# Optimization experiments

Hardware: AMD Instinct MI355X
Metric: run time of the kernel (lower is better)

Reference implementation:

```python
import jax, jax.numpy as jnp
import numpy as np

B = 1024; PAST = 64; FUT = 16; N = PAST + FUT; DM = N // 3; HID = 64
EMB = [(2000, 32), (7, 8), (24, 8)]
OUTP = 3 + 32 + 8 + 8  # 51 = out_preprocess
O = OUTP - 1           # 50
HID1 = 64; HID2 = 64
NEG = -1e30  # finite stand-in for -inf so fully-masked rows stay NaN-free


def _gcnn(x, A, W, act):
    # D = diag((1 + rowsum(sign(relu(A-1e-15))))^-0.5); out = act(D @ A @ D @ (x W^T))
    d = (1.0 + (A > 1e-15).astype(x.dtype).sum(1)) ** -0.5
    An = d[:, None] * A * d[None, :]            # (P,P)
    h = jnp.einsum('pq,bqc->bpc', An, x @ W.T)  # (B,P,out)
    return jax.nn.relu(h) if act else h


def _forward(data, emb0, emb1, emb2, w1, b1, w2, b2, w3, b3,
             M, Wg1a, Wg1b, Wk, smoothing, Wg2a, Wg2b):
    # learned adjacency: masked softmax over strictly-lower-triangular support
    mask = jnp.tril(jnp.ones((N, N), data.dtype), -1)
    A0 = jax.nn.relu(M @ M.T)
    A = jax.nn.softmax(jnp.where(mask > 0, A0, NEG), axis=1)
    A = jnp.where(mask > 0, A, 0.0)
    # pre_processing: embeddings + MLP, then re-append last raw column
    tabs = (emb0, emb1, emb2)
    e = [t[data[:, :, i].astype(jnp.int32)] for i, t in enumerate(tabs)]
    h = jnp.concatenate(e + [data[:, :, -3:]], -1)        # (B,N,51)
    h = jax.nn.relu(h @ w1.T + b1)
    h = jax.nn.relu(h @ w2.T + b2)
    h = h @ w3.T + b3                                      # (B,N,50)
    x = jnp.concatenate([h, data[:, :, -1:]], -1)          # (B,N,51)
    sg1, sg2 = x[:, :PAST], x[:, PAST:]
    A11 = A[:PAST, :PAST]
    x1 = _gcnn(_gcnn(sg1, A11, Wg1a, True), A11, Wg1b, False)   # (B,PAST,50)
    xk = jnp.concatenate([x1, sg2[:, :, :-1]], 1)               # (B,N,50)
    y = x[:, :PAST, -1:]                                        # (B,PAST,1)
    # Kernel: batched Mahalanobis quadratic form (diagonal computed directly)
    xp, xf = xk[:, :PAST], xk[:, PAST:]
    theta = Wk @ Wk.T
    theta = (theta + theta.T) / 2
    diff = xp[:, None, :, :] - xf[:, :, None, :]                # (B,F,P,50)
    q = jnp.einsum('bjip,pq,bjiq->bji', diff, theta, diff)      # (B,F,P)
    alpha = -0.5 * q / (jax.nn.sigmoid(smoothing[0]) * 0.01)
    At = A[FUT:, :PAST] if False else A[PAST:, :PAST]           # (F,P)
    At = jax.nn.softmax(jnp.where(At != 0, At, NEG), axis=1)
    # torch Softmax(dim=1) on (B,F,P) normalizes over the F axis
    alpha = jax.nn.softmax(jnp.where(At[None] >= 0.004, alpha, NEG), axis=1)
    yh = jnp.einsum('bjp,bpo->bjo', alpha, y)                   # (B,F,1)
    x2 = jnp.concatenate([sg2[:, :, :-1], yh], -1)              # (B,F,51)
    A22 = A[PAST:, PAST:]
    out = _gcnn(_gcnn(x2, A22, Wg2a, True), A22, Wg2b, False).reshape(-1, FUT)
    # cdist(x, x), p=2, with NaN-safe sqrt at zero distance
    xc = jnp.concatenate([sg1, x2], 1)                          # (B,N,51)
    sq = jnp.sum(xc * xc, -1)
    d2 = jnp.maximum(sq[:, :, None] + sq[:, None, :]
                     - 2.0 * jnp.einsum('bnc,bmc->bnm', xc, xc), 0.0)
    dist = jnp.where(d2 > 0, jnp.sqrt(jnp.where(d2 > 0, d2, 1.0)), 0.0)
    return (out, dist, A)


def setup_inputs() -> dict:
    key = jax.random.key(0)
    ks = jax.random.split(key, 20)
    cols = [jax.random.randint(ks[i], (B, N, 1), 0, EMB[i][0]).astype(jnp.float32)
            for i in range(3)]
    data = jnp.concatenate(cols + [jax.random.normal(ks[3], (B, N, 3), jnp.float32)], -1)
    g = lambda k, s, sc: jax.random.normal(k, s, jnp.float32) * sc
    return dict(
        data=data,
        emb0=g(ks[4], EMB[0], 1.0),
        emb1=g(ks[5], EMB[1], 1.0),
        emb2=g(ks[6], EMB[2], 1.0),
        w1=g(ks[7], (128, OUTP), OUTP ** -0.5), b1=jnp.zeros((128,), jnp.float32),
        w2=g(ks[8], (128, 128), 128 ** -0.5), b2=jnp.zeros((128,), jnp.float32),
        w3=g(ks[9], (O, 128), 128 ** -0.5), b3=jnp.zeros((O,), jnp.float32),
        M=g(ks[10], (N, DM), 1.0),
        Wg1a=g(ks[11], (HID1, OUTP), OUTP ** -0.5),
        Wg1b=g(ks[12], (O, HID1), HID1 ** -0.5),
        Wk=g(ks[13], (O, HID), 0.05),
        smoothing=g(ks[14], (1,), 1.0),
        Wg2a=g(ks[15], (HID2, OUTP), OUTP ** -0.5),
        Wg2b=g(ks[16], (1, HID2), HID2 ** -0.5),
    )


def reference(data, emb0, emb1, emb2, w1, b1, w2, b2, w3, b3,
              M, Wg1a, Wg1b, Wk, smoothing, Wg2a, Wg2b):
    return _forward(data, emb0, emb1, emb2, w1, b1, w2, b2, w3, b3,
                    M, Wg1a, Wg1b, Wk, smoothing, Wg2a, Wg2b)
```

## Files before the change

### kernel.cpp

```cpp
#include <hip/hip_runtime.h>
#include <math.h>


#define NEGBIG (-1e30f)

#define OFF_X     0
#define OFF_YH    7454720
#define OFF_A     7471104
#define OFF_AN22  7481600
#define OFF_MK    7484356
#define OFF_GAH   7514692
#define OFF_GAL   7516740
#define OFF_G2AT  7521156
#define OFF_SC    7524420
#define OFF_W1H   7524424
#define OFF_W1L   7528520
#define OFF_W2H   7532616
#define OFF_W2L   7540808
#define OFF_W3H   7549000
#define OFF_W3L   7553096
#define OFF_ANH   7557192
#define OFF_ANL   7559240
#define OFF_GBH   7561288
#define OFF_GBL   7563336
#define OFF_WKH   7565384
#define OFF_WKL   7567432

#define OUT_OUT   0
#define OUT_DIST  16384
#define OUT_A     6569984

typedef __attribute__((ext_vector_type(8))) short bf16x8;
typedef __attribute__((ext_vector_type(4))) short s16x4;
typedef __attribute__((ext_vector_type(4))) float f32x4;

__device__ __forceinline__ unsigned short f2bf(float x) {
  union { float f; unsigned u; } v; v.f = x;
  unsigned r = v.u + 0x7fffu + ((v.u >> 16) & 1u);
  return (unsigned short)(r >> 16);
}
__device__ __forceinline__ float bf2f(unsigned short h) {
  union { unsigned u; float f; } v; v.u = ((unsigned)h) << 16; return v.f;
}
__device__ __forceinline__ void split2(float v, unsigned short& h, unsigned short& l) {
  unsigned short hh = f2bf(v);
  h = hh;
  l = f2bf(v - bf2f(hh));
}
#define SWZ6(r, k) (((r) << 6) + (((((k) >> 3) ^ ((r) & 7)) << 3) | ((k) & 7)))
#define SWZ7(r, k) (((r) << 7) + (((((k) >> 3) ^ ((r) & 7)) << 3) | ((k) & 7)))

#define MFMA3(acc, aH, aL, bH, bL) \
  acc = __builtin_amdgcn_mfma_f32_16x16x32_bf16(aH, bH, acc, 0, 0, 0); \
  acc = __builtin_amdgcn_mfma_f32_16x16x32_bf16(aH, bL, acc, 0, 0, 0); \
  acc = __builtin_amdgcn_mfma_f32_16x16x32_bf16(aL, bH, acc, 0, 0, 0);
#define MFMA4(acc, aH, aL, bH, bL) \
  MFMA3(acc, aH, aL, bH, bL) \
  acc = __builtin_amdgcn_mfma_f32_16x16x32_bf16(aL, bL, acc, 0, 0, 0);

__global__ __launch_bounds__(256) void k_prep(
    const float* __restrict__ M, const float* __restrict__ Wk,
    const float* __restrict__ sm,
    const float* __restrict__ w1, const float* __restrict__ w2,
    const float* __restrict__ w3,
    const float* __restrict__ wg1a, const float* __restrict__ wg1b,
    const float* __restrict__ wg2a,
    float* __restrict__ ws, float* __restrict__ out)
{
  __shared__ float Msh[80 * 26];
  __shared__ float Ash[80 * 80];
  __shared__ float d1[64];
  __shared__ float d2s[16];
  const int t = threadIdx.x;

  if (blockIdx.x == 0) {
    for (int e = t; e < 80 * 26; e += 256) Msh[e] = M[e];
    __syncthreads();
    for (int e = t; e < 6400; e += 256) {
      int i = e / 80, j = e % 80;
      float v = 0.f;
      if (j < i) {
        float s = 0.f;
        for (int k = 0; k < 26; ++k) s += Msh[i * 26 + k] * Msh[j * 26 + k];
        v = s > 0.f ? s : 0.f;
      }
      Ash[e] = v;
    }
    __syncthreads();
    if (t > 0 && t < 80) {
      int i = t;
      float m = -3.4e38f;
      for (int j = 0; j < i; ++j) m = fmaxf(m, Ash[i * 80 + j]);
      float s = 0.f;
      for (int j = 0; j < i; ++j) {
        float e = expf(Ash[i * 80 + j] - m);
        Ash[i * 80 + j] = e;
        s += e;
      }
      float inv = 1.f / s;
      for (int j = 0; j < i; ++j) Ash[i * 80 + j] *= inv;
    }
    __syncthreads();
    {
      float* Aws = ws + OFF_A;
      float* Aout = out + OUT_A;
      for (int e = t; e < 6400; e += 256) { Aws[e] = Ash[e]; Aout[e] = Ash[e]; }
    }
    if (t < 64) {
      int c = 0;
      for (int j = 0; j < 64; ++j) if (Ash[t * 80 + j] > 1e-15f) ++c;
      d1[t] = 1.f / sqrtf(1.f + (float)c);
    } else if (t < 80) {
      int i = t - 64; int c = 0;
      for (int j = 0; j < 16; ++j) if (Ash[(64 + i) * 80 + 64 + j] > 1e-15f) ++c;
      d2s[i] = 1.f / sqrtf(1.f + (float)c);
    }
    __syncthreads();
    {
      float* an22 = ws + OFF_AN22;
      unsigned short* anH = (unsigned short*)(ws + OFF_ANH);
      unsigned short* anL = (unsigned short*)(ws + OFF_ANL);
      for (int e = t; e < 4096; e += 256) {
        int i = e >> 6, j = e & 63;
        float v = d1[i] * Ash[i * 80 + j] * d1[j];
        unsigned short h = f2bf(v);
        anH[e] = h; anL[e] = f2bf(v - bf2f(h));
      }
      for (int e = t; e < 256; e += 256) {
        int i = e >> 4, j = e & 15;
        an22[e] = d2s[i] * Ash[(64 + i) * 80 + 64 + j] * d2s[j];
      }
    }
    if (t < 16) {
      float* mk = ws + OFF_MK;
      int j = t;
      float m = -3.4e38f;
      for (int i = 0; i < 64; ++i) {
        float v = Ash[(64 + j) * 80 + i];
        v = (v != 0.f) ? v : NEGBIG;
        m = fmaxf(m, v);
      }
      float s = 0.f;
      for (int i = 0; i < 64; ++i) {
        float v = Ash[(64 + j) * 80 + i];
        v = (v != 0.f) ? v : NEGBIG;
        s += expf(v - m);
      }
      float inv = 1.f / s;
      for (int i = 0; i < 64; ++i) {
        float v = Ash[(64 + j) * 80 + i];
        v = (v != 0.f) ? v : NEGBIG;
        mk[j * 64 + i] = (expf(v - m) * inv >= 0.004f) ? 1.f : 0.f;
      }
    }
  } else if (blockIdx.x == 1) {
    unsigned short* wkh = (unsigned short*)(ws + OFF_WKH);
    unsigned short* wkl = (unsigned short*)(ws + OFF_WKL);
    for (int e = t; e < 4096; e += 256) {
      int h = e >> 6, o = e & 63;
      float v = (o < 50) ? Wk[o * 64 + h] : 0.f;
      unsigned short hh = f2bf(v);
      wkh[e] = hh; wkl[e] = f2bf(v - bf2f(hh));
    }
    if (t == 0) {
      float v = sm[0];
      float sig = 1.f / (1.f + expf(-v));
      (ws + OFF_SC)[0] = -0.5f / (sig * 0.01f);
    }
  } else if (blockIdx.x == 2) {
    unsigned short* w1h = (unsigned short*)(ws + OFF_W1H);
    unsigned short* w1l = (unsigned short*)(ws + OFF_W1L);
    for (int e = t; e < 8192; e += 256) {
      int n = e >> 6, k = e & 63;
      float v = (k < 51) ? w1[n * 51 + k] : 0.f;
      unsigned short h = f2bf(v);
      w1h[e] = h; w1l[e] = f2bf(v - bf2f(h));
    }
    unsigned short* w3h = (unsigned short*)(ws + OFF_W3H);
    unsigned short* w3l = (unsigned short*)(ws + OFF_W3L);
    for (int e = t; e < 8192; e += 256) {
      int n = e >> 7, k = e & 127;
      float v = (n < 50) ? w3[n * 128 + k] : 0.f;
      unsigned short h = f2bf(v);
      w3h[e] = h; w3l[e] = f2bf(v - bf2f(h));
    }
    unsigned short* gah = (unsigned short*)(ws + OFF_GAH);
    unsigned short* gal = (unsigned short*)(ws + OFF_GAL);
    for (int e = t; e < 4096; e += 256) {
      int n = e >> 6, k = e & 63;
      float v = (k < 51) ? wg1a[n * 51 + k] : 0.f;
      unsigned short h = f2bf(v);
      gah[e] = h; gal[e] = f2bf(v - bf2f(h));
    }
  } else {
    unsigned short* w2h = (unsigned short*)(ws + OFF_W2H);
    unsigned short* w2l = (unsigned short*)(ws + OFF_W2L);
    for (int e = t; e < 16384; e += 256) {
      int n = e >> 7, k = e & 127;
      float v = w2[n * 128 + k];
      unsigned short h = f2bf(v);
      w2h[e] = h; w2l[e] = f2bf(v - bf2f(h));
    }
    unsigned short* gbh = (unsigned short*)(ws + OFF_GBH);
    unsigned short* gbl = (unsigned short*)(ws + OFF_GBL);
    for (int e = t; e < 4096; e += 256) {
      int n = e >> 6, k = e & 63;
      float v = (n < 50) ? wg1b[n * 64 + k] : 0.f;
      unsigned short h = f2bf(v);
      gbh[e] = h; gbl[e] = f2bf(v - bf2f(h));
    }
    float* g2at = ws + OFF_G2AT;
    for (int e = t; e < 64 * 51; e += 256) { int o = e / 51, k = e % 51; g2at[k * 64 + o] = wg2a[e]; }
  }
}

__global__ __launch_bounds__(512) void k_mlp(
    const float* __restrict__ data,
    const float* __restrict__ emb0, const float* __restrict__ emb1,
    const float* __restrict__ emb2,
    const float* __restrict__ b1, const float* __restrict__ b2,
    const float* __restrict__ b3,
    float* __restrict__ ws)
{
  __shared__ __align__(16) unsigned short actH[64 * 128];
  __shared__ __align__(16) unsigned short actL[64 * 128];
  __shared__ __align__(16) unsigned short wbH[8192];
  __shared__ __align__(16) unsigned short wbL[8192];
  const int t = threadIdx.x;
  const int lane = t & 63, wave = t >> 6;
  const int s = wave & 3, half = wave >> 2;
  const int m16 = lane & 15, quad = lane >> 4;
  const int base = blockIdx.x * 64;
  const int row0 = s * 16;
  const int arow = row0 + m16;
  const unsigned short* w1h = (const unsigned short*)(ws + OFF_W1H);
  const unsigned short* w1l = (const unsigned short*)(ws + OFF_W1L);
  const unsigned short* w2h = (const unsigned short*)(ws + OFF_W2H);
  const unsigned short* w2l = (const unsigned short*)(ws + OFF_W2L);
  const unsigned short* w3h = (const unsigned short*)(ws + OFF_W3H);
  const unsigned short* w3l = (const unsigned short*)(ws + OFF_W3L);
  float* x = ws + OFF_X;

  for (int e = t; e < 4096; e += 512) {
    int r = e >> 6, c = e & 63;
    int g = base + r;
    float v = 0.f;
    if (c < 32)      { int i0 = (int)data[g * 6 + 0]; v = emb0[i0 * 32 + c]; }
    else if (c < 40) { int i1 = (int)data[g * 6 + 1]; v = emb1[i1 * 8 + (c - 32)]; }
    else if (c < 48) { int i2 = (int)data[g * 6 + 2]; v = emb2[i2 * 8 + (c - 40)]; }
    else if (c < 51) { v = data[g * 6 + 3 + (c - 48)]; }
    int idx = SWZ7(r, c);
    split2(v, actH[idx], actL[idx]);
  }
  for (int q = t; q < 1024; q += 512) {
    int col = q >> 3, c = q & 7;
    int dst = (col << 6) + ((c ^ (col & 7)) << 3);
    *(bf16x8*)(wbH + dst) = *(const bf16x8*)(w1h + (col << 6) + (c << 3));
    *(bf16x8*)(wbL + dst) = *(const bf16x8*)(w1l + (col << 6) + (c << 3));
  }
  bf16x8 pH[2], pL[2];
#pragma unroll
  for (int i = 0; i < 2; ++i) {
    int q = t + i * 512;
    int coll = q >> 4, c = q & 15;
    int src = (coll << 7) + (c << 3);
    pH[i] = *(const bf16x8*)(w2h + src);
    pL[i] = *(const bf16x8*)(w2l + src);
  }
  if (t < 64) x[(base + t) * 51 + 50] = data[(base + t) * 6 + 5];
  __syncthreads();

  {
    f32x4 acc[4];
#pragma unroll
    for (int n = 0; n < 4; ++n) acc[n] = (f32x4){0.f, 0.f, 0.f, 0.f};
#pragma unroll
    for (int kb8 = 0; kb8 < 8; kb8 += 4) {
      int ach = ((quad + kb8) ^ (m16 & 7)) << 3;
      bf16x8 aH = *(const bf16x8*)(actH + (arow << 7) + ach);
      bf16x8 aL = *(const bf16x8*)(actL + (arow << 7) + ach);
#pragma unroll
      for (int n = 0; n < 4; ++n) {
        const int col = (half * 4 + n) * 16 + m16;
        int boff = (col << 6) + ach;
        bf16x8 bH = *(const bf16x8*)(wbH + boff);
        bf16x8 bL = *(const bf16x8*)(wbL + boff);
        MFMA3(acc[n], aH, aL, bH, bL)
      }
    }
#pragma unroll
    for (int n = 0; n < 4; ++n) {
      const int col = (half * 4 + n) * 16 + m16;
      const float bias = b1[col];
#pragma unroll
      for (int r = 0; r < 4; ++r) {
        float v = acc[n][r] + bias; v = v > 0.f ? v : 0.f;
        int idx = SWZ7(row0 + quad * 4 + r, col);
        split2(v, actH[idx], actL[idx]);
      }
    }
  }
  __syncthreads();

#pragma unroll
  for (int i = 0; i < 2; ++i) {
    int q = t + i * 512;
    int coll = q >> 4, c = q & 15;
    int dst = (coll << 7) + ((c ^ (coll & 7)) << 3);
    *(bf16x8*)(wbH + dst) = pH[i];
    *(bf16x8*)(wbL + dst) = pL[i];
  }
#pragma unroll
  for (int i = 0; i < 2; ++i) {
    int q = t + i * 512;
    int coll = q >> 4, c = q & 15;
    int src = ((64 + coll) << 7) + (c << 3);
    pH[i] = *(const bf16x8*)(w2h + src);
    pL[i] = *(const bf16x8*)(w2l + src);
  }
  __syncthreads();

  f32x4 acc2[2][2];
#pragma unroll
  for (int a2 = 0; a2 < 2; ++a2)
#pragma unroll
    for (int n = 0; n < 2; ++n) acc2[a2][n] = (f32x4){0.f, 0.f, 0.f, 0.f};
#pragma unroll
  for (int kb8 = 0; kb8 < 16; kb8 += 4) {
    int ach = ((quad + kb8) ^ (m16 & 7)) << 3;
    bf16x8 aH = *(const bf16x8*)(actH + (arow << 7) + ach);
    bf16x8 aL = *(const bf16x8*)(actL + (arow << 7) + ach);
#pragma unroll
    for (int n = 0; n < 2; ++n) {
      const int cl = (half * 2 + n) * 16 + m16;
      int boff = (cl << 7) + ach;
      bf16x8 bH = *(const bf16x8*)(wbH + boff);
      bf16x8 bL = *(const bf16x8*)(wbL + boff);
      MFMA3(acc2[0][n], aH, aL, bH, bL)
    }
  }
  __syncthreads();

#pragma unroll
  for (int i = 0; i < 2; ++i) {
    int q = t + i * 512;
    int coll = q >> 4, c = q & 15;
    int dst = (coll << 7) + ((c ^ (coll & 7)) << 3);
    *(bf16x8*)(wbH + dst) = pH[i];
    *(bf16x8*)(wbL + dst) = pL[i];
  }
#pragma unroll
  for (int i = 0; i < 2; ++i) {
    int q = t + i * 512;
    int coll = q >> 4, c = q & 15;
    int src = (coll << 7) + (c << 3);
    pH[i] = *(const bf16x8*)(w3h + src);
    pL[i] = *(const bf16x8*)(w3l + src);
  }
  __syncthreads();

#pragma unroll
  for (int kb8 = 0; kb8 < 16; kb8 += 4) {
    int ach = ((quad + kb8) ^ (m16 & 7)) << 3;
    bf16x8 aH = *(const bf16x8*)(actH + (arow << 7) + ach);
    bf16x8 aL = *(const bf16x8*)(actL + (arow << 7) + ach);
#pragma unroll
    for (int n = 0; n < 2; ++n) {
      const int cl = (half * 2 + n) * 16 + m16;
      int boff = (cl << 7) + ach;
      bf16x8 bH = *(const bf16x8*)(wbH + boff);
      bf16x8 bL = *(const bf16x8*)(wbL + boff);
      MFMA3(acc2[1][n], aH, aL, bH, bL)
    }
  }
  __syncthreads();

#pragma unroll
  for (int hh = 0; hh < 2; ++hh) {
#pragma unroll
    for (int n = 0; n < 2; ++n) {
      const int col = hh * 64 + (half * 2 + n) * 16 + m16;
      const float bias = b2[col];
#pragma unroll
      for (int r = 0; r < 4; ++r) {
        float v = acc2[hh][n][r] + bias; v = v > 0.f ? v : 0.f;
        int idx = SWZ7(row0 + quad * 4 + r, col);
        split2(v, actH[idx], actL[idx]);
      }
    }
  }
#pragma unroll
  for (int i = 0; i < 2; ++i) {
    int q = t + i * 512;
    int coll = q >> 4, c = q & 15;
    int dst = (coll << 7) + ((c ^ (coll & 7)) << 3);
    *(bf16x8*)(wbH + dst) = pH[i];
    *(bf16x8*)(wbL + dst) = pL[i];
  }
  __syncthreads();

  {
    f32x4 acc[2];
#pragma unroll
    for (int n = 0; n < 2; ++n) acc[n] = (f32x4){0.f, 0.f, 0.f, 0.f};
#pragma unroll
    for (int kb8 = 0; kb8 < 16; kb8 += 4) {
      int ach = ((quad + kb8) ^ (m16 & 7)) << 3;
      bf16x8 aH = *(const bf16x8*)(actH + (arow << 7) + ach);
      bf16x8 aL = *(const bf16x8*)(actL + (arow << 7) + ach);
#pragma unroll
      for (int n = 0; n < 2; ++n) {
        const int col = (half * 2 + n) * 16 + m16;
        int boff = (col << 7) + ach;
        bf16x8 bH = *(const bf16x8*)(wbH + boff);
        bf16x8 bL = *(const bf16x8*)(wbL + boff);
        MFMA3(acc[n], aH, aL, bH, bL)
      }
    }
#pragma unroll
    for (int n = 0; n < 2; ++n) {
      const int col = (half * 2 + n) * 16 + m16;
      if (col < 50) {
        const float bias = b3[col];
#pragma unroll
        for (int r = 0; r < 4; ++r) {
          int row = row0 + quad * 4 + r;
          x[(base + row) * 51 + col] = acc[n][r] + bias;
        }
      }
    }
  }
}

__global__ __launch_bounds__(512) void k_gq(const float* __restrict__ wg2b,
                                            float* __restrict__ ws,
                                            float* __restrict__ out)
{
  __shared__ __align__(16) unsigned short SH[32768];
  unsigned short* b1H = SH;
  unsigned short* b1L = SH + 4096;
  unsigned short* b2H = SH + 8192;
  unsigned short* b2L = SH + 12288;
  unsigned short* anH = SH + 16384;
  unsigned short* anL = SH + 20480;
  unsigned short* wH  = SH + 24576;
  unsigned short* wL  = SH + 28672;
  unsigned short* xfH = SH + 24576;
  unsigned short* xfL = SH + 25600;
  unsigned short* zfH = SH + 26624;
  unsigned short* zfL = SH + 27648;
  float* alS  = (float*)(SH + 28672);
  float* spH2 = (float*)(SH + 30848);
  float* spS  = (float*)(SH + 31104);
  float* sfS  = (float*)(SH + 31232);
  float* yvS  = (float*)(SH + 31264);
  float* yhsS = (float*)(SH + 31392);
  float* X2v  = (float*)(SH + 8192);
  float* A22v = X2v + 832;
  float* G2v  = A22v + 256;
  float* Pmv  = G2v + 1024;
  float* wb2  = Pmv + 1024;
  float* zzv  = wb2 + 64;

  const int t = threadIdx.x, b = blockIdx.x;
  const int lane = t & 63, wave = t >> 6;
  const int s = wave & 3, half = wave >> 2;
  const int m16 = lane & 15, quad = lane >> 4;
  const int row0 = s * 16;
  const int arow = row0 + m16;
  const float* x = ws + OFF_X;
  const float* mk = ws + OFF_MK;
  const float* an22 = ws + OFF_AN22;
  const float* g2at = ws + OFF_G2AT;
  const unsigned short* gAnH = (const unsigned short*)(ws + OFF_ANH);
  const unsigned short* gAnL = (const unsigned short*)(ws + OFF_ANL);
  const unsigned short* gaH = (const unsigned short*)(ws + OFF_GAH);
  const unsigned short* gaL = (const unsigned short*)(ws + OFF_GAL);
  const unsigned short* gbH = (const unsigned short*)(ws + OFF_GBH);
  const unsigned short* gbL = (const unsigned short*)(ws + OFF_GBL);
  const unsigned short* gwkH = (const unsigned short*)(ws + OFF_WKH);
  const unsigned short* gwkL = (const unsigned short*)(ws + OFF_WKL);
  const float sc = (ws + OFF_SC)[0];
  float* yh = ws + OFF_YH;

  for (int e = t; e < 4096; e += 512) {
    int r = e >> 6, k = e & 63;
    float v = (k < 51) ? x[(b * 80 + r) * 51 + k] : 0.f;
    int idx = SWZ6(r, k);
    split2(v, b1H[idx], b1L[idx]);
  }
  {
    int q = t;
    if (q < 512) {
      int r = q >> 3, c = q & 7;
      int dst = (r << 6) + ((c ^ (r & 7)) << 3);
      int src = (r << 6) + (c << 3);
      *(bf16x8*)(anH + dst) = *(const bf16x8*)(gAnH + src);
      *(bf16x8*)(anL + dst) = *(const bf16x8*)(gAnL + src);
      *(bf16x8*)(wH + dst)  = *(const bf16x8*)(gaH + src);
      *(bf16x8*)(wL + dst)  = *(const bf16x8*)(gaL + src);
    }
  }
  float yvreg = 0.f;
  if (t < 64) yvreg = x[(b * 80 + t) * 51 + 50];
  bf16x8 pH, pL;
  {
    int q = t & 511;
    int r = q >> 3, c = q & 7;
    int src = (r << 6) + (c << 3);
    pH = *(const bf16x8*)(gbH + src);
    pL = *(const bf16x8*)(gbL + src);
  }
  __syncthreads();

  f32x4 accA[2];
#pragma unroll
  for (int n = 0; n < 2; ++n) accA[n] = (f32x4){0.f, 0.f, 0.f, 0.f};
#pragma unroll
  for (int kb8 = 0; kb8 < 8; kb8 += 4) {
    int ach = ((quad + kb8) ^ (m16 & 7)) << 3;
    bf16x8 aH = *(const bf16x8*)(b1H + (arow << 6) + ach);
    bf16x8 aL = *(const bf16x8*)(b1L + (arow << 6) + ach);
#pragma unroll
    for (int n = 0; n < 2; ++n) {
      const int col = (half * 2 + n) * 16 + m16;
      int boff = (col << 6) + ach;
      bf16x8 bH = *(const bf16x8*)(wH + boff);
      bf16x8 bL = *(const bf16x8*)(wL + boff);
      MFMA3(accA[n], aH, aL, bH, bL)
    }
  }
  __syncthreads();

  {
    const int kb = row0 + quad * 4;
#pragma unroll
    for (int n = 0; n < 2; ++n) {
      const int col = (half * 2 + n) * 16 + m16;
      int idx = (col << 6) + (((((kb >> 3) ^ (col & 7)) << 3)) | (kb & 7));
      s16x4 hv, lv;
#pragma unroll
      for (int r = 0; r < 4; ++r) {
        unsigned short hh, ll; split2(accA[n][r], hh, ll);
        hv[r] = (short)hh; lv[r] = (short)ll;
      }
      *(s16x4*)(b2H + idx) = hv; *(s16x4*)(b2L + idx) = lv;
    }
  }
  {
    int q = t & 511;
    int r = q >> 3, c = q & 7;
    int dst = (r << 6) + ((c ^ (r & 7)) << 3);
    *(bf16x8*)(wH + dst) = pH;
    *(bf16x8*)(wL + dst) = pL;
    int src = (r << 6) + (c << 3);
    pH = *(const bf16x8*)(gwkH + src);
    pL = *(const bf16x8*)(gwkL + src);
  }
  __syncthreads();

#pragma unroll
  for (int n = 0; n < 2; ++n) accA[n] = (f32x4){0.f, 0.f, 0.f, 0.f};
#pragma unroll
  for (int kb8 = 0; kb8 < 8; kb8 += 4) {
    int ach = ((quad + kb8) ^ (m16 & 7)) << 3;
    bf16x8 aH = *(const bf16x8*)(anH + (arow << 6) + ach);
    bf16x8 aL = *(const bf16x8*)(anL + (arow << 6) + ach);
#pragma unroll
    for (int n = 0; n < 2; ++n) {
      const int col = (half * 2 + n) * 16 + m16;
      int boff = (col << 6) + ach;
      bf16x8 bH = *(const bf16x8*)(b2H + boff);
      bf16x8 bL = *(const bf16x8*)(b2L + boff);
      MFMA3(accA[n], aH, aL, bH, bL)
    }
  }
  __syncthreads();

  {
    const int kb = row0 + quad * 4;
#pragma unroll
    for (int n = 0; n < 2; ++n) {
      const int col = (half * 2 + n) * 16 + m16;
      int idx = (col << 6) + (((((kb >> 3) ^ (col & 7)) << 3)) | (kb & 7));
      s16x4 hv, lv;
#pragma unroll
      for (int r = 0; r < 4; ++r) {
        float v = accA[n][r]; v = v > 0.f ? v : 0.f;
        unsigned short hh, ll; split2(v, hh, ll);
        hv[r] = (short)hh; lv[r] = (short)ll;
      }
      *(s16x4*)(b2H + idx) = hv; *(s16x4*)(b2L + idx) = lv;
    }
  }
  __syncthreads();

#pragma unroll
  for (int n = 0; n < 2; ++n) accA[n] = (f32x4){0.f, 0.f, 0.f, 0.f};
#pragma unroll
  for (int kb8 = 0; kb8 < 8; kb8 += 4) {
    int ach = ((quad + kb8) ^ (m16 & 7)) << 3;
    bf16x8 aH = *(const bf16x8*)(anH + (arow << 6) + ach);
    bf16x8 aL = *(const bf16x8*)(anL + (arow << 6) + ach);
#pragma unroll
    for (int n = 0; n < 2; ++n) {
      const int col = (half * 2 + n) * 16 + m16;
      int boff = (col << 6) + ach;
      bf16x8 bH = *(const bf16x8*)(b2H + boff);
      bf16x8 bL = *(const bf16x8*)(b2L + boff);
      MFMA3(accA[n], aH, aL, bH, bL)
    }
  }
  __syncthreads();

#pragma unroll
  for (int n = 0; n < 2; ++n) {
    const int col = (half * 2 + n) * 16 + m16;
#pragma unroll
    for (int r = 0; r < 4; ++r) {
      int idx = SWZ6(row0 + quad * 4 + r, col);
      split2(accA[n][r], b1H[idx], b1L[idx]);
    }
  }
  {
    int q = t & 511;
    int r = q >> 3, c = q & 7;
    int dst = (r << 6) + ((c ^ (r & 7)) << 3);
    *(bf16x8*)(anH + dst) = pH;
    *(bf16x8*)(anL + dst) = pL;
  }
  float xf0 = 0.f, xf1 = 0.f;
  {
    int e0 = t, e1 = t + 512;
    int r0r = e0 >> 6, c0 = e0 & 63;
    int r1r = e1 >> 6, c1 = e1 & 63;
    if (c0 < 50) xf0 = x[(b * 80 + 64 + r0r) * 51 + c0];
    if (c1 < 50) xf1 = x[(b * 80 + 64 + r1r) * 51 + c1];
  }
  __syncthreads();

#pragma unroll
  for (int n = 0; n < 2; ++n) accA[n] = (f32x4){0.f, 0.f, 0.f, 0.f};
#pragma unroll
  for (int kb8 = 0; kb8 < 8; kb8 += 4) {
    int ach = ((quad + kb8) ^ (m16 & 7)) << 3;
    bf16x8 aH = *(const bf16x8*)(b1H + (arow << 6) + ach);
    bf16x8 aL = *(const bf16x8*)(b1L + (arow << 6) + ach);
#pragma unroll
    for (int n = 0; n < 2; ++n) {
      const int col = (half * 2 + n) * 16 + m16;
      int boff = (col << 6) + ach;
      bf16x8 bH = *(const bf16x8*)(wH + boff);
      bf16x8 bL = *(const bf16x8*)(wL + boff);
      MFMA3(accA[n], aH, aL, bH, bL)
    }
  }
  __syncthreads();

#pragma unroll
  for (int n = 0; n < 2; ++n) {
    const int col = (half * 2 + n) * 16 + m16;
#pragma unroll
    for (int r = 0; r < 4; ++r) {
      int idx = SWZ6(row0 + quad * 4 + r, col);
      split2(accA[n][r], b2H[idx], b2L[idx]);
    }
  }
  {
    int e0 = t, e1 = t + 512;
    int i0 = SWZ6(e0 >> 6, e0 & 63);
    int i1 = SWZ6(e1 >> 6, e1 & 63);
    split2(xf0, xfH[i0], xfL[i0]);
    split2(xf1, xfH[i1], xfL[i1]);
  }
  if (t < 64) yvS[t] = yvreg;
  __syncthreads();

#pragma unroll
  for (int n = 0; n < 2; ++n) accA[n] = (f32x4){0.f, 0.f, 0.f, 0.f};
#pragma unroll
  for (int kb8 = 0; kb8 < 8; kb8 += 4) {
    int ach = ((quad + kb8) ^ (m16 & 7)) << 3;
    bf16x8 aH = *(const bf16x8*)(b2H + (arow << 6) + ach);
    bf16x8 aL = *(const bf16x8*)(b2L + (arow << 6) + ach);
#pragma unroll
    for (int n = 0; n < 2; ++n) {
      const int col = (half * 2 + n) * 16 + m16;
      int boff = (col << 6) + ach;
      bf16x8 bH = *(const bf16x8*)(anH + boff);
      bf16x8 bL = *(const bf16x8*)(anL + boff);
      MFMA4(accA[n], aH, aL, bH, bL)
    }
  }
  if (half == 0) {
    f32x4 af = (f32x4){0.f, 0.f, 0.f, 0.f};
#pragma unroll
    for (int kb8 = 0; kb8 < 8; kb8 += 4) {
      int ach = ((quad + kb8) ^ (m16 & 7)) << 3;
      bf16x8 aH = *(const bf16x8*)(xfH + (m16 << 6) + ach);
      bf16x8 aL = *(const bf16x8*)(xfL + (m16 << 6) + ach);
      const int col = s * 16 + m16;
      int boff = (col << 6) + ach;
      bf16x8 bH = *(const bf16x8*)(anH + boff);
      bf16x8 bL = *(const bf16x8*)(anL + boff);
      MFMA4(af, aH, aL, bH, bL)
    }
    const int h = s * 16 + m16;
#pragma unroll
    for (int r = 0; r < 4; ++r) {
      int idx = SWZ6(quad * 4 + r, h);
      split2(af[r], zfH[idx], zfL[idx]);
    }
  }
  {
    float s2[4];
#pragma unroll
    for (int r = 0; r < 4; ++r)
      s2[r] = accA[0][r] * accA[0][r] + accA[1][r] * accA[1][r];
#pragma unroll
    for (int n = 0; n < 2; ++n) {
      const int h = (half * 2 + n) * 16 + m16;
#pragma unroll
      for (int r = 0; r < 4; ++r) {
        int idx = SWZ6(row0 + quad * 4 + r, h);
        split2(accA[n][r], b1H[idx], b1L[idx]);
      }
    }
#pragma unroll
    for (int m = 1; m < 16; m <<= 1)
#pragma unroll
      for (int r = 0; r < 4; ++r) s2[r] += __shfl_xor(s2[r], m);
    if (m16 == 0) {
#pragma unroll
      for (int r = 0; r < 4; ++r)
        spH2[(row0 + quad * 4 + r) * 2 + half] = s2[r];
    }
  }
  __syncthreads();

  if (t < 64) {
    spS[t] = spH2[t * 2] + spH2[t * 2 + 1];
  } else if (t < 80) {
    int j = t - 64;
    float ssum = 0.f;
    for (int h = 0; h < 64; ++h) {
      int idx = SWZ6(j, h);
      float v = bf2f(zfH[idx]) + bf2f(zfL[idx]);
      ssum += v * v;
    }
    sfS[j] = ssum;
  }
  __syncthreads();

  {
    f32x4 ac2 = (f32x4){0.f, 0.f, 0.f, 0.f};
#pragma unroll
    for (int kb8 = 0; kb8 < 8; kb8 += 4) {
      int ach = ((quad + kb8) ^ (m16 & 7)) << 3;
      bf16x8 aH = *(const bf16x8*)(b1H + (arow << 6) + ach);
      bf16x8 aL = *(const bf16x8*)(b1L + (arow << 6) + ach);
      bf16x8 bH = *(const bf16x8*)(zfH + (m16 << 6) + ach);
      bf16x8 bL = *(const bf16x8*)(zfL + (m16 << 6) + ach);
      MFMA4(ac2, aH, aL, bH, bL)
    }
    if (half == 0) {
#pragma unroll
      for (int r = 0; r < 4; ++r) {
        int i = row0 + quad * 4 + r;
        alS[i * 17 + m16] = sc * (spS[i] + sfS[m16] - 2.f * ac2[r]);
      }
    }
  }
  __syncthreads();

  if (t < 64) {
    const int i = t;
    float lv[16];
    float m = -3.4e38f;
#pragma unroll
    for (int j = 0; j < 16; ++j) {
      float v = (mk[j * 64 + i] != 0.f) ? alS[i * 17 + j] : NEGBIG;
      lv[j] = v;
      m = fmaxf(m, v);
    }
    float ssum = 0.f;
#pragma unroll
    for (int j = 0; j < 16; ++j) { lv[j] = expf(lv[j] - m); ssum += lv[j]; }
    float inv = 1.f / ssum;
#pragma unroll
    for (int j = 0; j < 16; ++j) alS[i * 17 + j] = lv[j] * inv;
  }
  __syncthreads();

  if (t < 16) {
    float ssum = 0.f;
    for (int i = 0; i < 64; ++i) ssum += alS[i * 17 + t] * yvS[i];
    yh[b * 16 + t] = ssum;
    yhsS[t] = ssum;
  }
  __syncthreads();

  for (int e = t; e < 832; e += 512) {
    int r = e / 52, c = e - r * 52;
    float v = 0.f;
    if (c < 50)       v = x[(b * 80 + 64 + r) * 51 + c];
    else if (c == 50) v = yhsS[r];
    X2v[e] = v;
  }
  for (int e = t; e < 256; e += 512) A22v[e] = an22[e];
  if (t < 64) wb2[t] = wg2b[t];
  __syncthreads();
  for (int e = t; e < 1024; e += 512) {
    int j = e >> 6, h = e & 63;
    float ssum = 0.f;
    for (int k = 0; k < 51; ++k) ssum += X2v[j * 52 + k] * g2at[k * 64 + h];
    G2v[e] = ssum;
  }
  __syncthreads();
  for (int e = t; e < 1024; e += 512) {
    int j = e >> 6, h = e & 63;
    float ssum = 0.f;
#pragma unroll
    for (int k = 0; k < 16; ++k) ssum += A22v[j * 16 + k] * G2v[k * 64 + h];
    Pmv[e] = ssum > 0.f ? ssum : 0.f;
  }
  __syncthreads();
  if (t < 16) {
    float ssum = 0.f;
    for (int h = 0; h < 64; ++h) ssum += Pmv[t * 64 + h] * wb2[h];
    zzv[t] = ssum;
  }
  __syncthreads();
  if (t < 16) {
    float ssum = 0.f;
#pragma unroll
    for (int k = 0; k < 16; ++k) ssum += A22v[t * 16 + k] * zzv[k];
    out[OUT_OUT + b * 16 + t] = ssum;
  }
}

__global__ __launch_bounds__(320) void k_dist(float* __restrict__ ws,
                                              float* __restrict__ out)
{
  __shared__ __align__(16) unsigned short xcH[5120], xcL[5120];
  __shared__ float sq[80];
  const int t = threadIdx.x, b = blockIdx.x;
  const int lane = t & 63, wave = t >> 6;
  const int m16 = lane & 15, quad = lane >> 4;
  const int row0 = wave * 16;
  const int arow = row0 + m16;
  const float* x = ws + OFF_X;
  const float* yhg = ws + OFF_YH;
  float* dist = out + OUT_DIST + b * 6400;

  for (int e = t; e < 5120; e += 320) {
    int n = e >> 6, c = e & 63;
    float v = 0.f;
    if (c < 50)       v = x[(b * 80 + n) * 51 + c];
    else if (c == 50) v = (n < 64) ? x[(b * 80 + n) * 51 + 50] : yhg[b * 16 + (n - 64)];
    int idx = SWZ6(n, c);
    split2(v, xcH[idx], xcL[idx]);
  }
  __syncthreads();

  f32x4 acc[5];
#pragma unroll
  for (int n = 0; n < 5; ++n) acc[n] = (f32x4){0.f, 0.f, 0.f, 0.f};
#pragma unroll
  for (int kb8 = 0; kb8 < 8; kb8 += 4) {
    int ach = ((quad + kb8) ^ (m16 & 7)) << 3;
    bf16x8 aH = *(const bf16x8*)(xcH + (arow << 6) + ach);
    bf16x8 aL = *(const bf16x8*)(xcL + (arow << 6) + ach);
#pragma unroll
    for (int nf = 0; nf < 5; ++nf) {
      const int col = nf * 16 + m16;
      int boff = (col << 6) + ach;
      bf16x8 bH = *(const bf16x8*)(xcH + boff);
      bf16x8 bL = *(const bf16x8*)(xcL + boff);
      MFMA3(acc[nf], aH, aL, bH, bL)
    }
  }
  if ((m16 >> 2) == quad) sq[row0 + m16] = acc[wave][m16 & 3];
  __syncthreads();

#pragma unroll
  for (int nf = 0; nf < 5; ++nf) {
    const int m = nf * 16 + m16;
#pragma unroll
    for (int r = 0; r < 4; ++r) {
      int i = row0 + quad * 4 + r;
      float d2 = sq[i] + sq[m] - 2.f * acc[nf][r];
      d2 = d2 > 0.f ? d2 : 0.f;
      dist[i * 80 + m] = d2 > 0.f ? sqrtf(d2) : 0.f;
    }
  }
}

extern "C" void kernel_launch(void* const* d_in, const int* in_sizes, int n_in,
                              void* d_out, int out_size, void* d_ws, size_t ws_size,
                              hipStream_t stream)
{
  const float* data = (const float*)d_in[0];
  const float* emb0 = (const float*)d_in[1];
  const float* emb1 = (const float*)d_in[2];
  const float* emb2 = (const float*)d_in[3];
  const float* w1   = (const float*)d_in[4];
  const float* b1   = (const float*)d_in[5];
  const float* w2   = (const float*)d_in[6];
  const float* b2   = (const float*)d_in[7];
  const float* w3   = (const float*)d_in[8];
  const float* b3   = (const float*)d_in[9];
  const float* M    = (const float*)d_in[10];
  const float* wg1a = (const float*)d_in[11];
  const float* wg1b = (const float*)d_in[12];
  const float* Wk   = (const float*)d_in[13];
  const float* smo  = (const float*)d_in[14];
  const float* wg2a = (const float*)d_in[15];
  const float* wg2b = (const float*)d_in[16];
  float* ws  = (float*)d_ws;
  float* out = (float*)d_out;

  k_prep<<<dim3(4),    dim3(256), 0, stream>>>(M, Wk, smo, w1, w2, w3, wg1a, wg1b, wg2a, ws, out);
  k_mlp <<<dim3(1280), dim3(512), 0, stream>>>(data, emb0, emb1, emb2, b1, b2, b3, ws);
  k_gq  <<<dim3(1024), dim3(512), 0, stream>>>(wg2b, ws, out);
  k_dist<<<dim3(1024), dim3(320), 0, stream>>>(ws, out);
}
```

Before: 213.6 us.

## Fuse pairwise distance computation into the gq kernel and drop yh workspace

New measurement: 210.3 us. About the same (-1.5%).

```diff
diff --git a/kernel.cpp b/kernel.cpp
--- a/kernel.cpp
+++ b/kernel.cpp
@@ -5,7 +5,6 @@
 #define NEGBIG (-1e30f)
 
 #define OFF_X     0
-#define OFF_YH    7454720
 #define OFF_A     7471104
 #define OFF_AN22  7481600
 #define OFF_MK    7484356
@@ -432,9 +431,9 @@
   }
 }
 
-__global__ __launch_bounds__(512) void k_gq(const float* __restrict__ wg2b,
-                                            float* __restrict__ ws,
-                                            float* __restrict__ out)
+__global__ __launch_bounds__(512) void k_gqd(const float* __restrict__ wg2b,
+                                             float* __restrict__ ws,
+                                             float* __restrict__ out)
 {
   __shared__ __align__(16) unsigned short SH[32768];
   unsigned short* b1H = SH;
@@ -461,6 +460,9 @@
   float* Pmv  = G2v + 1024;
   float* wb2  = Pmv + 1024;
   float* zzv  = wb2 + 64;
+  unsigned short* xcH = SH;
+  unsigned short* xcL = SH + 16384;
+  float* sqS = (float*)(SH + 21504);
 
   const int t = threadIdx.x, b = blockIdx.x;
   const int lane = t & 63, wave = t >> 6;
@@ -481,7 +483,6 @@
   const unsigned short* gwkH = (const unsigned short*)(ws + OFF_WKH);
   const unsigned short* gwkL = (const unsigned short*)(ws + OFF_WKL);
   const float sc = (ws + OFF_SC)[0];
-  float* yh = ws + OFF_YH;
 
   for (int e = t; e < 4096; e += 512) {
     int r = e >> 6, k = e & 63;
@@ -795,11 +796,18 @@
   if (t < 16) {
     float ssum = 0.f;
     for (int i = 0; i < 64; ++i) ssum += alS[i * 17 + t] * yvS[i];
-    yh[b * 16 + t] = ssum;
     yhsS[t] = ssum;
   }
   __syncthreads();
 
+  for (int e = t; e < 5120; e += 512) {
+    int n = e >> 6, c = e & 63;
+    float v = 0.f;
+    if (c < 50)       v = x[(b * 80 + n) * 51 + c];
+    else if (c == 50) v = (n < 64) ? x[(b * 80 + n) * 51 + 50] : yhsS[n - 64];
+    int idx = SWZ6(n, c);
+    split2(v, xcH[idx], xcL[idx]);
+  }
   for (int e = t; e < 832; e += 512) {
     int r = e / 52, c = e - r * 52;
     float v = 0.f;
@@ -810,6 +818,28 @@
   for (int e = t; e < 256; e += 512) A22v[e] = an22[e];
   if (t < 64) wb2[t] = wg2b[t];
   __syncthreads();
+
+  f32x4 accD[4];
+  {
+    int tc = 0;
+    for (int idx = wave; idx < 25; idx += 8) {
+      int ts = idx / 5, tf = idx - ts * 5;
+      f32x4 acc = (f32x4){0.f, 0.f, 0.f, 0.f};
+#pragma unroll
+      for (int kb8 = 0; kb8 < 8; kb8 += 4) {
+        int ach = ((quad + kb8) ^ (m16 & 7)) << 3;
+        bf16x8 aH = *(const bf16x8*)(xcH + ((ts * 16 + m16) << 6) + ach);
+        bf16x8 aL = *(const bf16x8*)(xcL + ((ts * 16 + m16) << 6) + ach);
+        const int col = tf * 16 + m16;
+        int boff = (col << 6) + ach;
+        bf16x8 bH = *(const bf16x8*)(xcH + boff);
+        bf16x8 bL = *(const bf16x8*)(xcL + boff);
+        MFMA3(acc, aH, aL, bH, bL)
+      }
+      if (ts == tf && (m16 >> 2) == quad) sqS[ts * 16 + m16] = acc[m16 & 3];
+      accD[tc++] = acc;
+    }
+  }
   for (int e = t; e < 1024; e += 512) {
     int j = e >> 6, h = e & 63;
     float ssum = 0.f;
@@ -817,12 +847,29 @@
     G2v[e] = ssum;
   }
   __syncthreads();
+
   for (int e = t; e < 1024; e += 512) {
     int j = e >> 6, h = e & 63;
     float ssum = 0.f;
 #pragma unroll
     for (int k = 0; k < 16; ++k) ssum += A22v[j * 16 + k] * G2v[k * 64 + h];
     Pmv[e] = ssum > 0.f ? ssum : 0.f;
+  }
+  {
+    float* dist = out + OUT_DIST + b * 6400;
+    int tc = 0;
+    for (int idx = wave; idx < 25; idx += 8) {
+      int ts = idx / 5, tf = idx - ts * 5;
+      f32x4 acc = accD[tc++];
+#pragma unroll
+      for (int r = 0; r < 4; ++r) {
+        int i = ts * 16 + quad * 4 + r;
+        int m = tf * 16 + m16;
+        float d2 = sqS[i] + sqS[m] - 2.f * acc[r];
+        d2 = d2 > 0.f ? d2 : 0.f;
+        dist[i * 80 + m] = d2 > 0.f ? sqrtf(d2) : 0.f;
+      }
+    }
   }
   __syncthreads();
   if (t < 16) {
@@ -836,63 +883,6 @@
 #pragma unroll
     for (int k = 0; k < 16; ++k) ssum += A22v[t * 16 + k] * zzv[k];
     out[OUT_OUT + b * 16 + t] = ssum;
-  }
-}
-
-__global__ __launch_bounds__(320) void k_dist(float* __restrict__ ws,
-                                              float* __restrict__ out)
-{
-  __shared__ __align__(16) unsigned short xcH[5120], xcL[5120];
-  __shared__ float sq[80];
-  const int t = threadIdx.x, b = blockIdx.x;
-  const int lane = t & 63, wave = t >> 6;
-  const int m16 = lane & 15, quad = lane >> 4;
-  const int row0 = wave * 16;
-  const int arow = row0 + m16;
-  const float* x = ws + OFF_X;
-  const float* yhg = ws + OFF_YH;
-  float* dist = out + OUT_DIST + b * 6400;
-
-  for (int e = t; e < 5120; e += 320) {
-    int n = e >> 6, c = e & 63;
-    float v = 0.f;
-    if (c < 50)       v = x[(b * 80 + n) * 51 + c];
-    else if (c == 50) v = (n < 64) ? x[(b * 80 + n) * 51 + 50] : yhg[b * 16 + (n - 64)];
-    int idx = SWZ6(n, c);
-    split2(v, xcH[idx], xcL[idx]);
-  }
-  __syncthreads();
-
-  f32x4 acc[5];
-#pragma unroll
-  for (int n = 0; n < 5; ++n) acc[n] = (f32x4){0.f, 0.f, 0.f, 0.f};
-#pragma unroll
-  for (int kb8 = 0; kb8 < 8; kb8 += 4) {
-    int ach = ((quad + kb8) ^ (m16 & 7)) << 3;
-    bf16x8 aH = *(const bf16x8*)(xcH + (arow << 6) + ach);
-    bf16x8 aL = *(const bf16x8*)(xcL + (arow << 6) + ach);
-#pragma unroll
-    for (int nf = 0; nf < 5; ++nf) {
-      const int col = nf * 16 + m16;
-      int boff = (col << 6) + ach;
-      bf16x8 bH = *(const bf16x8*)(xcH + boff);
-      bf16x8 bL = *(const bf16x8*)(xcL + boff);
-      MFMA3(acc[nf], aH, aL, bH, bL)
-    }
-  }
-  if ((m16 >> 2) == quad) sq[row0 + m16] = acc[wave][m16 & 3];
-  __syncthreads();
-
-#pragma unroll
-  for (int nf = 0; nf < 5; ++nf) {
-    const int m = nf * 16 + m16;
-#pragma unroll
-    for (int r = 0; r < 4; ++r) {
-      int i = row0 + quad * 4 + r;
-      float d2 = sq[i] + sq[m] - 2.f * acc[nf][r];
-      d2 = d2 > 0.f ? d2 : 0.f;
-      dist[i * 80 + m] = d2 > 0.f ? sqrtf(d2) : 0.f;
-    }
   }
 }
 
@@ -922,6 +912,5 @@
 
   k_prep<<<dim3(4),    dim3(256), 0, stream>>>(M, Wk, smo, w1, w2, w3, wg1a, wg1b, wg2a, ws, out);
   k_mlp <<<dim3(1280), dim3(512), 0, stream>>>(data, emb0, emb1, emb2, b1, b2, b3, ws);
-  k_gq  <<<dim3(1024), dim3(512), 0, stream>>>(wg2b, ws, out);
-  k_dist<<<dim3(1024), dim3(320), 0, stream>>>(ws, out);
+  k_gqd <<<dim3(1024), dim3(512), 0, stream>>>(wg2b, ws, out);
 }
```
